# Kernel tuning notes

Hardware: AMD Instinct MI355X
Metric: run time of the kernel (lower is better)

## Reference

```python
import jax, jax.numpy as jnp
import numpy as np
from jax import lax

RANK = 2
INPUT_SIZE = 8
HIDDEN_SIZE = 1024
NUM_MIXTURES = 4
ALPHA = 0.1
BASE_SCALE = 500.0
D = 2 * RANK + INPUT_SIZE  # 12
BATCH, SEQ_LEN = 64, 512


def setup_inputs() -> dict:
    key = jax.random.key(0)
    k1, k2, k3, k4, k5 = jax.random.split(key, 5)
    return {
        "x": jax.random.normal(k1, (BATCH, SEQ_LEN, INPUT_SIZE), jnp.float32),
        "eps": jax.random.normal(k2, (NUM_MIXTURES, HIDDEN_SIZE, D), jnp.float32),
        "means": jax.random.normal(k3, (NUM_MIXTURES, D), jnp.float32),
        "scale_tril_raw": jax.random.normal(k4, (NUM_MIXTURES, D, D), jnp.float32) / np.sqrt(HIDDEN_SIZE),
        "mixture_weights": jax.random.uniform(k5, (NUM_MIXTURES,), jnp.float32),
    }


def reference(x, eps, means, scale_tril_raw, mixture_weights):
    # _clamp_tril: lower-triangular with strictly positive diagonal
    diag = jnp.abs(jnp.diagonal(scale_tril_raw, axis1=-2, axis2=-1) - 1e-12) + 1e-12  # [K,D]
    L = jnp.tril(scale_tril_raw, -1) + diag[..., None] * jnp.eye(D, dtype=scale_tril_raw.dtype)
    # _normalize_weights
    w = jnp.clip(mixture_weights, 1e-6, None)
    w = w / jnp.sum(w)
    # rsample: mean + eps @ L^T, per mixture -> [K, H, D]
    samp = means[:, None, :] + jnp.einsum('khd,ked->khe', eps, L)
    mixed = jnp.einsum('k,khd->hd', w, samp)  # weighted sum over mixtures [H, D]
    m = mixed[:, :RANK]            # [H, r]
    n = mixed[:, RANK:2 * RANK]    # [H, r]
    I = mixed[:, 2 * RANK:]        # [H, input_size]
    J = (m @ n.T) * (BASE_SCALE / HIDDEN_SIZE)  # [H, H]
    span = jnp.concatenate([m, I], axis=1)      # [H, r + input_size]

    def step(h, x_t):
        dh = -h + jnp.tanh(h) @ J.T + x_t @ I.T
        h_new = h + ALPHA * dh
        return h_new, h_new

    h0 = jnp.zeros((x.shape[0], HIDDEN_SIZE), x.dtype)
    _, hs = lax.scan(step, h0, jnp.swapaxes(x, 0, 1))  # hs: [T, B, H]
    hiddens = jnp.swapaxes(hs, 0, 1)                   # [B, T, H]
    pinv = jnp.linalg.pinv(span)                       # [r+input_size, H]
    return jnp.einsum('dh,bth->btd', pinv, hiddens)    # [B, T, r+input_size]
```

## Files before the change

### kernel.cpp

```cpp
#include <hip/hip_runtime.h>

#define HS   1024
#define SEQ  512
#define NBAT 64
#define INSZ 8
#define NM   4
#define DD   12
#define WV   8

#define ALPHA 0.1f
#define OMA   0.9f
#define SCL   (500.0f/1024.0f)
#define AS    (ALPHA*SCL)

#if __has_builtin(__builtin_amdgcn_exp2f)
  #define GSC 2.8853900817779268f
  #define EXPG(v) __builtin_amdgcn_exp2f(v)
#else
  #define GSC 2.0f
  #define EXPG(v) __expf(v)
#endif

typedef float f2 __attribute__((ext_vector_type(2)));
typedef float f4 __attribute__((ext_vector_type(4)));
__device__ __forceinline__ f2 mk2(float a, float b){ f2 r; r.x=a; r.y=b; return r; }
__device__ __forceinline__ f2 splat2(float a){ return mk2(a,a); }
#if __has_builtin(__builtin_elementwise_fma)
__device__ __forceinline__ f2 fma2(f2 a, f2 b, f2 c){ return __builtin_elementwise_fma(a,b,c); }
#else
__device__ __forceinline__ f2 fma2(f2 a, f2 b, f2 c){
  f2 r; r.x=fmaf(a.x,b.x,c.x); r.y=fmaf(a.y,b.y,c.y); return r; }
#endif

#define DPP_ADD(v, ctrl, rmask, bmask) \
  v += __int_as_float(__builtin_amdgcn_update_dpp(0, __float_as_int(v), ctrl, rmask, bmask, true))

__device__ __forceinline__ void wave64_sum2(float &a, float &b){
  DPP_ADD(a, 0x111, 0xf, 0xf); DPP_ADD(b, 0x111, 0xf, 0xf);
  DPP_ADD(a, 0x112, 0xf, 0xf); DPP_ADD(b, 0x112, 0xf, 0xf);
  DPP_ADD(a, 0x114, 0xf, 0xe); DPP_ADD(b, 0x114, 0xf, 0xe);
  DPP_ADD(a, 0x118, 0xf, 0xc); DPP_ADD(b, 0x118, 0xf, 0xc);
  DPP_ADD(a, 0x142, 0xa, 0xf); DPP_ADD(b, 0x142, 0xa, 0xf);
  DPP_ADD(a, 0x143, 0xc, 0xf); DPP_ADD(b, 0x143, 0xc, 0xf);
}

__device__ __forceinline__ void mix_unit(int i, const float* __restrict__ eps,
                                         const float* __restrict__ means,
                                         const float* __restrict__ tril,
                                         const float* w, float* outm){
  float ep[NM][DD];
  #pragma unroll
  for (int k=0;k<NM;k++){
    const float4* p = (const float4*)(eps + (size_t)(k*HS + i)*DD);
    float4 r0=p[0], r1=p[1], r2=p[2];
    ep[k][0]=r0.x; ep[k][1]=r0.y; ep[k][2]=r0.z; ep[k][3]=r0.w;
    ep[k][4]=r1.x; ep[k][5]=r1.y; ep[k][6]=r1.z; ep[k][7]=r1.w;
    ep[k][8]=r2.x; ep[k][9]=r2.y; ep[k][10]=r2.z; ep[k][11]=r2.w;
  }
  #pragma unroll
  for (int e=0;e<DD;e++){
    float a = 0.f;
    #pragma unroll
    for (int k=0;k<NM;k++){
      float se = means[k*DD+e];
      #pragma unroll
      for (int d=0; d<e; d++) se = fmaf(ep[k][d], tril[(k*DD+e)*DD+d], se);
      float dg = fabsf(tril[(k*DD+e)*DD+e] - 1e-12f) + 1e-12f;
      se = fmaf(ep[k][e], dg, se);
      a = fmaf(w[k], se, a);
    }
    outm[e] = a;
  }
}

__global__ __launch_bounds__(512,1)
void rnn_scan(const float* __restrict__ x, const float* __restrict__ eps,
              const float* __restrict__ means, const float* __restrict__ tril,
              const float* __restrict__ mw, float* __restrict__ out)
{
  const int b    = blockIdx.x;
  const int tid  = threadIdx.x;
  const int wave = tid >> 6;
  const int lane = tid & 63;

  __shared__ float xs[SEQ*INSZ];
  __shared__ __align__(16) f2 red[2][WV];
  __shared__ __align__(16) float outb[SEQ*10];

  { const f4* xp=(const f4*)(x + (size_t)b*SEQ*INSZ);
    f4* xd=(f4*)xs;
    for (int idx=tid; idx<SEQ*INSZ/4; idx+=512) xd[idx]=xp[idx]; }

  float w[NM];
  { float s=0.f;
    #pragma unroll
    for (int k=0;k<NM;k++){ w[k]=fmaxf(mw[k],1e-6f); s+=w[k]; }
    float inv=1.0f/s;
    #pragma unroll
    for (int k=0;k<NM;k++) w[k]*=inv; }

  f2 m0g, m1g, n0v, n1v, I2[8];
  float pn0, pn1;
  {
    float mmA[DD], mmB[DD];
    mix_unit(tid,       eps, means, tril, w, mmA);
    mix_unit(tid + 512, eps, means, tril, w, mmB);
    m0g = mk2((GSC*AS)*mmA[0], (GSC*AS)*mmB[0]);
    m1g = mk2((GSC*AS)*mmA[1], (GSC*AS)*mmB[1]);
    n0v = mk2(-2.f*mmA[2],     -2.f*mmB[2]);
    n1v = mk2(-2.f*mmA[3],     -2.f*mmB[3]);
    pn0 = mmA[2]+mmB[2];
    pn1 = mmA[3]+mmB[3];
    #pragma unroll
    for (int e=0;e<8;e++) I2[e] = mk2(mmA[4+e], mmB[4+e]);
  }

  wave64_sum2(pn0, pn1);
  if (lane==63) red[0][wave] = mk2(pn0,pn1);
  __syncthreads();
  float N0, N1;
  { const f4* rq = (const f4*)&red[0][0];
    f4 Q0=rq[0], Q1=rq[1], Q2=rq[2], Q3=rq[3];
    f4 S = (Q0+Q1)+(Q2+Q3);
    N0 = S.x + S.z;  N1 = S.y + S.w; }
  __syncthreads();

  const float ALG = GSC*ALPHA;
  f2 hs = mk2(0.f,0.f);
  float o = 0.f;

  const f4* xs4 = (const f4*)xs;
  f4 xa = xs4[0], xb = xs4[1];

  #pragma unroll 2
  for (int t=0;t<SEQ;t++){
    float e0=EXPG(hs.x), e1=EXPG(hs.y);
    f2 rq = mk2(__builtin_amdgcn_rcpf(e0+1.f), __builtin_amdgcn_rcpf(e1+1.f));
    f2 s0 = rq*n0v, s1 = rq*n1v;
    float u0 = s0.x+s0.y, u1 = s1.x+s1.y;
    wave64_sum2(u0,u1);
    if (lane==63) red[t&1][wave] = mk2(u0,u1);

    f2 inj;
    { f2 a =      I2[0]*splat2(xa.x);
      a = fma2(I2[1], splat2(xa.y), a);
      a = fma2(I2[2], splat2(xa.z), a);
      a = fma2(I2[3], splat2(xa.w), a);
      a = fma2(I2[4], splat2(xb.x), a);
      a = fma2(I2[5], splat2(xb.y), a);
      a = fma2(I2[6], splat2(xb.z), a);
      a = fma2(I2[7], splat2(xb.w), a);
      inj = a; }
    f2 hpre = fma2(splat2(OMA), hs, inj*splat2(ALG));
    { const int tn = (t+1)&(SEQ-1); xa = xs4[tn*2]; xb = xs4[tn*2+1]; }

    __syncthreads();
    float U0, U1;
    { const f4* rr = (const f4*)&red[t&1][0];
      f4 Q0=rr[0], Q1=rr[1], Q2=rr[2], Q3=rr[3];
      f4 S = (Q0+Q1)+(Q2+Q3);
      U0 = N0 + (S.x + S.z);
      U1 = N1 + (S.y + S.w); }

    hs = fma2(m0g, splat2(U0), fma2(m1g, splat2(U1), hpre));

    if (tid < 10){
      float add = (tid==0) ? SCL*U0 : (tid==1) ? SCL*U1 : xs[t*8 + tid-2];
      o = __builtin_fmaf(OMA, o, ALPHA*add);
      outb[t*10+tid] = o;
    }
  }

  __syncthreads();
  const f4* ob4 = (const f4*)outb;
  f4* o4 = (f4*)out + (size_t)b*(SEQ*10/4);
  for (int idx=tid; idx<SEQ*10/4; idx+=512) o4[idx]=ob4[idx];
}

extern "C" void kernel_launch(void* const* d_in, const int* in_sizes, int n_in,
                              void* d_out, int out_size, void* d_ws, size_t ws_size,
                              hipStream_t stream) {
  const float* x     = (const float*)d_in[0];
  const float* eps   = (const float*)d_in[1];
  const float* means = (const float*)d_in[2];
  const float* tril  = (const float*)d_in[3];
  const float* mw    = (const float*)d_in[4];
  float* out = (float*)d_out;

  rnn_scan<<<NBAT, 512, 0, stream>>>(x, eps, means, tril, mw, out);
}
```

Before: 270.5 us.

## Precompute input-injection trajectory in a parallel GEMM and run single-wave scan

Because the input term is linear, a separate kernel precomputes its contribution to each hidden unit's pre-activation for every timestep (a 64x512x1024 float tensor in workspace). A second kernel then runs the recurrence with one wave per batch: the rank-2 state lives in scalars, reductions use DPP plus readlane, and the per-step block barrier and LDS exchange are gone. The precomputed tensor is streamed into LDS with double-buffered global_load_lds. The cost is about 128 MB of extra global write and read traffic and only 64 waves of parallelism for the scan. The old kernel stays as a fallback when no workspace is provided.

```diff
diff --git a/kernel.cpp b/kernel.cpp
--- a/kernel.cpp
+++ b/kernel.cpp
@@ -6,6 +6,7 @@
 #define INSZ 8
 #define NM   4
 #define DD   12
+#define CHK  8
 #define WV   8
 
 #define ALPHA 0.1f
@@ -14,10 +15,10 @@
 #define AS    (ALPHA*SCL)
 
 #if __has_builtin(__builtin_amdgcn_exp2f)
-  #define GSC 2.8853900817779268f
+  #define GS 2.8853900817779268f
   #define EXPG(v) __builtin_amdgcn_exp2f(v)
 #else
-  #define GSC 2.0f
+  #define GS 2.0f
   #define EXPG(v) __expf(v)
 #endif
 
@@ -43,7 +44,9 @@
   DPP_ADD(a, 0x142, 0xa, 0xf); DPP_ADD(b, 0x142, 0xa, 0xf);
   DPP_ADD(a, 0x143, 0xc, 0xf); DPP_ADD(b, 0x143, 0xc, 0xf);
 }
-
+#define RD63(v) __int_as_float(__builtin_amdgcn_readlane(__float_as_int(v), 63))
+
+template<int E0, int E1>
 __device__ __forceinline__ void mix_unit(int i, const float* __restrict__ eps,
                                          const float* __restrict__ means,
                                          const float* __restrict__ tril,
@@ -58,7 +61,7 @@
     ep[k][8]=r2.x; ep[k][9]=r2.y; ep[k][10]=r2.z; ep[k][11]=r2.w;
   }
   #pragma unroll
-  for (int e=0;e<DD;e++){
+  for (int e=E0;e<E1;e++){
     float a = 0.f;
     #pragma unroll
     for (int k=0;k<NM;k++){
@@ -69,14 +72,196 @@
       se = fmaf(ep[k][e], dg, se);
       a = fmaf(w[k], se, a);
     }
-    outm[e] = a;
-  }
+    outm[e-E0] = a;
+  }
+}
+
+__device__ __forceinline__ void norm_w(const float* __restrict__ mw, float* w){
+  float s=0.f;
+  #pragma unroll
+  for (int k=0;k<NM;k++){ w[k]=fmaxf(mw[k],1e-6f); s+=w[k]; }
+  float inv=1.0f/s;
+  #pragma unroll
+  for (int k=0;k<NM;k++) w[k]*=inv;
+}
+
+__global__ __launch_bounds__(256,1)
+void gemm_c(const float* __restrict__ x, const float* __restrict__ eps,
+            const float* __restrict__ means, const float* __restrict__ tril,
+            const float* __restrict__ mw, float* __restrict__ C)
+{
+  const int b = blockIdx.x >> 2, q = blockIdx.x & 3;
+  const int tid = threadIdx.x;
+  __shared__ float xs[SEQ*INSZ];
+  __shared__ float yb[128][8];
+
+  float w[NM]; norm_w(mw, w);
+
+  float I[4][8];
+  #pragma unroll
+  for (int j=0;j<4;j++) mix_unit<4,12>(tid*4+j, eps, means, tril, w, I[j]);
+
+  { const float4* xp=(const float4*)(x + (size_t)b*SEQ*INSZ);
+    float4* xd=(float4*)xs;
+    for (int idx=tid; idx<SEQ*INSZ/4; idx+=256) xd[idx]=xp[idx]; }
+  __syncthreads();
+
+  if (tid < 8){
+    float Y=0.f; const int t0=q*128, tend=t0+128;
+    for (int t=0;t<tend;t++){
+      if (t>=t0) yb[t-t0][tid]=Y;
+      Y = fmaf(OMA, Y, (GS*ALPHA)*xs[t*8+tid]);
+    }
+  }
+  __syncthreads();
+
+  float* Cb = C + ((size_t)b*SEQ + (size_t)q*128)*HS + tid*4;
+  for (int tt=0; tt<128; tt++){
+    float4 ya=((float4*)yb[tt])[0], yc=((float4*)yb[tt])[1];
+    float cv[4];
+    #pragma unroll
+    for (int j=0;j<4;j++){
+      float a =       I[j][0]*ya.x;
+      a = fmaf(I[j][1],ya.y,a); a = fmaf(I[j][2],ya.z,a); a = fmaf(I[j][3],ya.w,a);
+      a = fmaf(I[j][4],yc.x,a); a = fmaf(I[j][5],yc.y,a);
+      a = fmaf(I[j][6],yc.z,a); a = fmaf(I[j][7],yc.w,a);
+      cv[j]=a;
+    }
+    *(float4*)(Cb + (size_t)tt*HS) = make_float4(cv[0],cv[1],cv[2],cv[3]);
+  }
+}
+
+#if __has_builtin(__builtin_amdgcn_global_load_lds)
+#define HAVE_GLLDS 1
+__device__ __forceinline__ void gl_lds16(const float* g, void* l){
+  __builtin_amdgcn_global_load_lds(
+      (const __attribute__((address_space(1))) unsigned int*)g,
+      (__attribute__((address_space(3))) unsigned int*)l, 16, 0, 0);
+}
+#endif
+
+__global__ __launch_bounds__(64,1)
+void rnn_scan1w(const float* __restrict__ x, const float* __restrict__ eps,
+                const float* __restrict__ means, const float* __restrict__ tril,
+                const float* __restrict__ mw, float* __restrict__ out,
+                const float* __restrict__ Cws)
+{
+  const int b    = blockIdx.x;
+  const int lane = threadIdx.x;
+
+  __shared__ float xs[SEQ*INSZ];
+  __shared__ f4    Pb[2][CHK][4][64];
+  __shared__ __align__(16) float outb[SEQ*10];
+
+  { const f4* xp=(const f4*)(x + (size_t)b*SEQ*INSZ);
+    f4* xd=(f4*)xs;
+    for (int idx=lane; idx<SEQ*INSZ/4; idx+=64) xd[idx]=xp[idx]; }
+
+  float w[NM]; norm_w(mw, w);
+
+  f2 m0v[8], m1v[8], n0v[8], n1v[8];
+  float sn0=0.f, sn1=0.f;
+  #pragma unroll
+  for (int jg=0;jg<4;jg++){
+    #pragma unroll
+    for (int c=0;c<4;c++){
+      float mm[4];
+      mix_unit<0,4>((jg*64+lane)*4+c, eps, means, tril, w, mm);
+      const int p = 2*jg + (c>>1);
+      if ((c&1)==0){ m0v[p].x=mm[0]; m1v[p].x=mm[1];
+                     n0v[p].x=-2.f*mm[2]; n1v[p].x=-2.f*mm[3]; }
+      else         { m0v[p].y=mm[0]; m1v[p].y=mm[1];
+                     n0v[p].y=-2.f*mm[2]; n1v[p].y=-2.f*mm[3]; }
+      sn0 += mm[2]; sn1 += mm[3];
+    }
+  }
+  wave64_sum2(sn0, sn1);
+  const float N0 = RD63(sn0), N1 = RD63(sn1);
+
+  __syncthreads();
+
+#ifdef HAVE_GLLDS
+  #define ISSUE(cc, bb) { \
+    const float* srcp = Cws + (size_t)(b*SEQ + (cc)*CHK)*HS + lane*4; \
+    _Pragma("unroll") for (int tt=0;tt<CHK;tt++) \
+      _Pragma("unroll") for (int jg=0;jg<4;jg++) \
+        gl_lds16(srcp + tt*HS + jg*256, (void*)&Pb[bb][tt][jg][0]); }
+#else
+  #define ISSUE(cc, bb) { \
+    const float* srcp = Cws + (size_t)(b*SEQ + (cc)*CHK)*HS + lane*4; \
+    _Pragma("unroll") for (int tt=0;tt<CHK;tt++) \
+      _Pragma("unroll") for (int jg=0;jg<4;jg++) \
+        Pb[bb][tt][jg][lane] = *(const f4*)(srcp + tt*HS + jg*256); }
+#endif
+
+  ISSUE(0, 0)
+
+  const float CA = GS*AS;
+  float A=0.f, Bst=0.f, o=0.f;
+
+  #define STEP(T, TN, buf, c0,c1,c2,c3, d0,d1,d2,d3) { \
+    d0=Pb[buf][TN][0][lane]; d1=Pb[buf][TN][1][lane]; \
+    d2=Pb[buf][TN][2][lane]; d3=Pb[buf][TN][3][lane]; \
+    f2 g[8]; \
+    g[0]=mk2(c0.x,c0.y); g[1]=mk2(c0.z,c0.w); \
+    g[2]=mk2(c1.x,c1.y); g[3]=mk2(c1.z,c1.w); \
+    g[4]=mk2(c2.x,c2.y); g[5]=mk2(c2.z,c2.w); \
+    g[6]=mk2(c3.x,c3.y); g[7]=mk2(c3.z,c3.w); \
+    { f2 A2=splat2(A), B2=splat2(Bst); \
+      _Pragma("unroll") for (int p=0;p<8;p++){ \
+        g[p]=fma2(m0v[p],A2,g[p]); g[p]=fma2(m1v[p],B2,g[p]); } } \
+    f2 rr[8]; \
+    _Pragma("unroll") for (int p=0;p<8;p++){ \
+      f2 ex = mk2(EXPG(g[p].x), EXPG(g[p].y)); \
+      f2 dd = mk2(ex.x+1.f, ex.y+1.f); \
+      rr[p] = mk2(__builtin_amdgcn_rcpf(dd.x), __builtin_amdgcn_rcpf(dd.y)); } \
+    f2 ua=mk2(0.f,0.f), ub=mk2(0.f,0.f), uc=mk2(0.f,0.f), ud=mk2(0.f,0.f); \
+    _Pragma("unroll") for (int p=0;p<4;p++){ ua=fma2(rr[p],n0v[p],ua); ub=fma2(rr[p],n1v[p],ub); } \
+    _Pragma("unroll") for (int p=4;p<8;p++){ uc=fma2(rr[p],n0v[p],uc); ud=fma2(rr[p],n1v[p],ud); } \
+    float u0=(ua.x+ua.y)+(uc.x+uc.y); \
+    float u1=(ub.x+ub.y)+(ud.x+ud.y); \
+    wave64_sum2(u0,u1); \
+    float U0 = N0 + RD63(u0); \
+    float U1 = N1 + RD63(u1); \
+    A   = fmaf(CA, U0, OMA*A); \
+    Bst = fmaf(CA, U1, OMA*Bst); \
+    if (lane<10){ \
+      float add = lane==0 ? SCL*U0 : lane==1 ? SCL*U1 : xs[(T)*8+lane-2]; \
+      o = fmaf(OMA, o, ALPHA*add); \
+      outb[(T)*10+lane]=o; } \
+  }
+
+  #pragma unroll 1
+  for (int c=0;c<SEQ/CHK;c++){
+    asm volatile("s_waitcnt vmcnt(0) lgkmcnt(0)" ::: "memory");
+#if __has_builtin(__builtin_amdgcn_sched_barrier)
+    __builtin_amdgcn_sched_barrier(0);
+#endif
+    if (c+1 < SEQ/CHK) ISSUE(c+1, (c+1)&1)
+    const int buf = c&1;
+    const int t0  = c*CHK;
+    f4 cA0=Pb[buf][0][0][lane], cA1=Pb[buf][0][1][lane],
+       cA2=Pb[buf][0][2][lane], cA3=Pb[buf][0][3][lane];
+    f4 cB0,cB1,cB2,cB3;
+    #pragma unroll 1
+    for (int tt=0; tt<CHK; tt+=2){
+      STEP(t0+tt,   tt+1,           buf, cA0,cA1,cA2,cA3, cB0,cB1,cB2,cB3)
+      STEP(t0+tt+1, (tt+2)&(CHK-1), buf, cB0,cB1,cB2,cB3, cA0,cA1,cA2,cA3)
+    }
+  }
+  #undef STEP
+  #undef ISSUE
+
+  __syncthreads();
+  const f4* ob4 = (const f4*)outb;
+  f4* o4 = (f4*)out + (size_t)b*(SEQ*10/4);
+  for (int idx=lane; idx<SEQ*10/4; idx+=64) o4[idx]=ob4[idx];
 }
 
 __global__ __launch_bounds__(512,1)
-void rnn_scan(const float* __restrict__ x, const float* __restrict__ eps,
-              const float* __restrict__ means, const float* __restrict__ tril,
-              const float* __restrict__ mw, float* __restrict__ out)
+void rnn_scan_fb(const float* __restrict__ x, const float* __restrict__ eps,
+                 const float* __restrict__ means, const float* __restrict__ tril,
+                 const float* __restrict__ mw, float* __restrict__ out)
 {
   const int b    = blockIdx.x;
   const int tid  = threadIdx.x;
@@ -91,24 +276,18 @@
     f4* xd=(f4*)xs;
     for (int idx=tid; idx<SEQ*INSZ/4; idx+=512) xd[idx]=xp[idx]; }
 
-  float w[NM];
-  { float s=0.f;
-    #pragma unroll
-    for (int k=0;k<NM;k++){ w[k]=fmaxf(mw[k],1e-6f); s+=w[k]; }
-    float inv=1.0f/s;
-    #pragma unroll
-    for (int k=0;k<NM;k++) w[k]*=inv; }
+  float w[NM]; norm_w(mw, w);
 
   f2 m0g, m1g, n0v, n1v, I2[8];
   float pn0, pn1;
   {
     float mmA[DD], mmB[DD];
-    mix_unit(tid,       eps, means, tril, w, mmA);
-    mix_unit(tid + 512, eps, means, tril, w, mmB);
-    m0g = mk2((GSC*AS)*mmA[0], (GSC*AS)*mmB[0]);
-    m1g = mk2((GSC*AS)*mmA[1], (GSC*AS)*mmB[1]);
-    n0v = mk2(-2.f*mmA[2],     -2.f*mmB[2]);
-    n1v = mk2(-2.f*mmA[3],     -2.f*mmB[3]);
+    mix_unit<0,12>(tid,       eps, means, tril, w, mmA);
+    mix_unit<0,12>(tid + 512, eps, means, tril, w, mmB);
+    m0g = mk2((GS*AS)*mmA[0], (GS*AS)*mmB[0]);
+    m1g = mk2((GS*AS)*mmA[1], (GS*AS)*mmB[1]);
+    n0v = mk2(-2.f*mmA[2],    -2.f*mmB[2]);
+    n1v = mk2(-2.f*mmA[3],    -2.f*mmB[3]);
     pn0 = mmA[2]+mmB[2];
     pn1 = mmA[3]+mmB[3];
     #pragma unroll
@@ -125,7 +304,7 @@
     N0 = S.x + S.z;  N1 = S.y + S.w; }
   __syncthreads();
 
-  const float ALG = GSC*ALPHA;
+  const float ALG = GS*ALPHA;
   f2 hs = mk2(0.f,0.f);
   float o = 0.f;
 
@@ -187,5 +366,12 @@
   const float* mw    = (const float*)d_in[4];
   float* out = (float*)d_out;
 
-  rnn_scan<<<NBAT, 512, 0, stream>>>(x, eps, means, tril, mw, out);
-}
+  const size_t cbytes = (size_t)NBAT*SEQ*HS*sizeof(float);
+  if (d_ws && ws_size >= cbytes){
+    gemm_c<<<NBAT*4, 256, 0, stream>>>(x, eps, means, tril, mw, (float*)d_ws);
+    rnn_scan1w<<<NBAT, 64, 0, stream>>>(x, eps, means, tril, mw, out,
+                                        (const float*)d_ws);
+  } else {
+    rnn_scan_fb<<<NBAT, 512, 0, stream>>>(x, eps, means, tril, mw, out);
+  }
+}
```

Result: slower. 394.9 us (+46.0%).
